# Kernel tuning notes

Measured on AMD Instinct MI355X. Metric: run time of the kernel, lower is better.

The kernel has to match this reference:

```python
import jax, jax.numpy as jnp
import numpy as np

B = 8192
D_LS, D_A, D_LM, D_AT, D_DS, D_DM = 1024, 512, 512, 512, 1024, 512
LENGTH = D_LS + D_A + D_LM  # 2048
OUT = 512


def setup_inputs() -> dict:
    key = jax.random.key(0)
    ks = jax.random.split(key, 9)
    return {
        "result_ls": jax.random.normal(ks[0], (B, 1, D_LS), jnp.float32),
        "result_A": jax.random.normal(ks[1], (B, 1, D_A), jnp.float32),
        "result_lm": jax.random.normal(ks[2], (B, 1, D_LM), jnp.float32),
        "result_AT": jax.random.normal(ks[3], (B, 1, D_AT), jnp.float32),
        "result_ds": jax.random.normal(ks[4], (B, 1, D_DS), jnp.float32),
        "result_dm": jax.random.normal(ks[5], (B, 1, D_DM), jnp.float32),
        "W": jax.random.normal(ks[6], (OUT, LENGTH), jnp.float32) * (1.0 / np.sqrt(LENGTH)),
        "b": jax.random.normal(ks[7], (OUT,), jnp.float32) * 0.01,
        "h_n": jax.random.normal(ks[8], (OUT, 1), jnp.float32) * (1.0 / np.sqrt(OUT)),
    }


def _pad_to(x, length):
    # zero-pad last dim of [B,1,d] to [B,1,length]
    return jnp.pad(x, ((0, 0), (0, 0), (0, length - x.shape[2])))


def reference(result_ls, result_A, result_lm, result_AT, result_ds, result_dm, W, b, h_n):
    # pad each node-type feature to common length and stack along node axis -> [B,6,L]
    nodes = jnp.concatenate(
        [_pad_to(t, LENGTH) for t in (result_ls, result_A, result_lm, result_AT, result_ds, result_dm)],
        axis=1,
    )
    temp = jnp.tanh(jnp.einsum("bnl,ol->bno", nodes, W) + b)  # [B,6,OUT]
    score = jnp.einsum("bno,oi->bni", temp, h_n)               # [B,6,1]
    score = score.reshape(-1, 1, 6)
    beta = jax.nn.softmax(score, axis=2)                        # [B,1,6]
    z_i = jnp.matmul(beta, nodes)                               # [B,1,L]
    return z_i
```

## Files before the change

### kernel.cpp

```cpp
#include <hip/hip_runtime.h>
#include <hip/hip_bf16.h>
#include <stdint.h>

typedef __attribute__((ext_vector_type(8))) short bf16x8;
typedef __attribute__((ext_vector_type(4))) float f32x4;

#define NB 8192

__device__ __forceinline__ unsigned pkbf(float x, float y) {
    __hip_bfloat162 h = __float22bfloat162_rn(make_float2(x, y));
    unsigned r;
    __builtin_memcpy(&r, &h, 4);
    return r;
}

__device__ __forceinline__ uint4 pack8(float4 a, float4 b) {
    uint4 r;
    r.x = pkbf(a.x, a.y);
    r.y = pkbf(a.z, a.w);
    r.z = pkbf(b.x, b.y);
    r.w = pkbf(b.z, b.w);
    return r;
}

__device__ __forceinline__ void gload_lds16(const float* g, void* l) {
    __builtin_amdgcn_global_load_lds(
        (const __attribute__((address_space(1))) void*)g,
        (__attribute__((address_space(3))) void*)l, 16, 0, 0);
}

__global__ __launch_bounds__(256)
void prep_w_kernel(const float* __restrict__ W, uint4* __restrict__ Wt) {
    int t = blockIdx.x * 256 + threadIdx.x;
    int lane = t & 63;
    int frag = t >> 6;
    int kb = frag >> 5, cb = frag & 31;
    int o = cb * 16 + (lane & 15);
    int k = kb * 32 + ((lane >> 4) << 3);
    const float* src = W + (size_t)o * 2048 + k;
    float4 a = *(const float4*)src;
    float4 b = *(const float4*)(src + 4);
    Wt[t] = pack8(a, b);
}

__global__ __launch_bounds__(512, 4)
void score_kernel(const float* __restrict__ x0, const float* __restrict__ x1,
                  const float* __restrict__ x2, const float* __restrict__ x3,
                  const float* __restrict__ x4, const float* __restrict__ x5,
                  const float* __restrict__ bias, const float* __restrict__ hvec,
                  const uint4* __restrict__ Wt, float* __restrict__ scores) {
    __shared__ uint4 lA[2][1024];
    __shared__ float red[8][64];

    int bid = blockIdx.x;
    int node = bid % 6;
    int tile = bid / 6;
    const float* xp; int dn;
    switch (node) {
        case 0: xp = x0; dn = 1024; break;
        case 1: xp = x1; dn = 512;  break;
        case 2: xp = x2; dn = 512;  break;
        case 3: xp = x3; dn = 512;  break;
        case 4: xp = x4; dn = 1024; break;
        default: xp = x5; dn = 512; break;
    }
    int m0 = tile * 64;
    int t = threadIdx.x;
    int lane = t & 63;
    int w = t >> 6;

    int nst = dn >> 6;

    int ra = ((w << 1) + 0) * 4 + (lane >> 4);
    int rb = ((w << 1) + 1) * 4 + (lane >> 4);
    int sa = (lane & 15) ^ (ra & 7);
    int sb = (lane & 15) ^ (rb & 7);
    const float* ga = xp + (size_t)(m0 + ra) * dn + (sa << 2);
    const float* gb = xp + (size_t)(m0 + rb) * dn + (sb << 2);
    char* lbaseA = (char*)&lA[0][0] + (((w << 1) + 0) << 10);
    char* lbaseB = (char*)&lA[0][0] + (((w << 1) + 1) << 10);

    gload_lds16(ga, lbaseA);
    gload_lds16(gb, lbaseB);
    ga += 64; gb += 64;
    __syncthreads();

    f32x4 acc[4][4];
#pragma unroll
    for (int mf = 0; mf < 4; ++mf)
#pragma unroll
        for (int nf = 0; nf < 4; ++nf)
            acc[mf][nf] = (f32x4){0.f, 0.f, 0.f, 0.f};

    const char* ldsroot = (const char*)&lA[0][0];

    for (int s = 0; s < nst; ++s) {
        int cur = s & 1;
        if (s + 1 < nst) {
            gload_lds16(ga, lbaseA + ((cur ^ 1) << 14));
            gload_lds16(gb, lbaseB + ((cur ^ 1) << 14));
            ga += 64; gb += 64;
        }
#pragma unroll
        for (int ks = 0; ks < 2; ++ks) {
            int kblock = (s << 1) + ks;
            const uint4* wp = Wt + (((kblock << 5) + (w << 2)) << 6) + lane;
            bf16x8 bfr[4];
#pragma unroll
            for (int nf = 0; nf < 4; ++nf) {
                uint4 u = wp[nf << 6];
                __builtin_memcpy(&bfr[nf], &u, 16);
            }
#pragma unroll
            for (int mf = 0; mf < 4; ++mf) {
                int r = (mf << 4) + (lane & 15);
                int slot = (ks << 3) + ((lane >> 4) << 1);
                int sw = r & 7;
                const char* p = ldsroot + (cur << 14) + (r << 8);
                float4 lo = *(const float4*)(p + (((slot) ^ sw) << 4));
                float4 hi = *(const float4*)(p + (((slot + 1) ^ sw) << 4));
                uint4 pk = pack8(lo, hi);
                bf16x8 afr;
                __builtin_memcpy(&afr, &pk, 16);
#pragma unroll
                for (int nf = 0; nf < 4; ++nf)
                    acc[mf][nf] = __builtin_amdgcn_mfma_f32_16x16x32_bf16(
                        afr, bfr[nf], acc[mf][nf], 0, 0, 0);
            }
        }
        __syncthreads();
    }

    float bv[4], hv[4];
#pragma unroll
    for (int nf = 0; nf < 4; ++nf) {
        int o = (w << 6) + (nf << 4) + (lane & 15);
        bv[nf] = bias[o];
        hv[nf] = hvec[o];
    }
#pragma unroll
    for (int mf = 0; mf < 4; ++mf) {
        float sc[4] = {0.f, 0.f, 0.f, 0.f};
#pragma unroll
        for (int nf = 0; nf < 4; ++nf) {
#pragma unroll
            for (int r = 0; r < 4; ++r) {
                float xv = acc[mf][nf][r] + bv[nf];
                float th = 1.f - 2.f * __builtin_amdgcn_rcpf(1.f + __expf(2.f * xv));
                sc[r] = fmaf(hv[nf], th, sc[r]);
            }
        }
#pragma unroll
        for (int r = 0; r < 4; ++r) {
            float v = sc[r];
            v += __shfl_xor(v, 1);
            v += __shfl_xor(v, 2);
            v += __shfl_xor(v, 4);
            v += __shfl_xor(v, 8);
            if ((lane & 15) == 0)
                red[w][(mf << 4) + ((lane >> 4) << 2) + r] = v;
        }
    }
    __syncthreads();
    if (t < 64) {
        float ssum = 0.f;
#pragma unroll
        for (int w2 = 0; w2 < 8; ++w2) ssum += red[w2][t];
        scores[node * NB + m0 + t] = ssum;
    }
}

__global__ __launch_bounds__(256)
void z_kernel(const float* __restrict__ x0, const float* __restrict__ x1,
              const float* __restrict__ x2, const float* __restrict__ x3,
              const float* __restrict__ x4, const float* __restrict__ x5,
              const float* __restrict__ scores, float* __restrict__ out) {
    int wv = threadIdx.x >> 6;
    int lane = threadIdx.x & 63;
    int b = (blockIdx.x << 2) + wv;

    float s0 = scores[b];
    float s1 = scores[NB + b];
    float s2 = scores[2 * NB + b];
    float s3 = scores[3 * NB + b];
    float s4 = scores[4 * NB + b];
    float s5 = scores[5 * NB + b];
    float m = fmaxf(fmaxf(fmaxf(s0, s1), fmaxf(s2, s3)), fmaxf(s4, s5));
    float e0 = __expf(s0 - m), e1 = __expf(s1 - m), e2 = __expf(s2 - m);
    float e3 = __expf(s3 - m), e4 = __expf(s4 - m), e5 = __expf(s5 - m);
    float inv = __builtin_amdgcn_rcpf(e0 + e1 + e2 + e3 + e4 + e5);
    float b0 = e0 * inv, b1 = e1 * inv, b2 = e2 * inv;
    float b3 = e3 * inv, b4 = e4 * inv, b5 = e5 * inv;

    const float* pls = x0 + (size_t)b * 1024;
    const float* pA  = x1 + (size_t)b * 512;
    const float* plm = x2 + (size_t)b * 512;
    const float* pAT = x3 + (size_t)b * 512;
    const float* pds = x4 + (size_t)b * 1024;
    const float* pdm = x5 + (size_t)b * 512;
    float* po = out + (size_t)b * 2048;

#pragma unroll
    for (int j = 0; j < 2; ++j) {
        int c = (j << 8) + (lane << 2);
        float4 vls = *(const float4*)(pls + c);
        float4 vA  = *(const float4*)(pA + c);
        float4 vlm = *(const float4*)(plm + c);
        float4 vAT = *(const float4*)(pAT + c);
        float4 vds = *(const float4*)(pds + c);
        float4 vdm = *(const float4*)(pdm + c);
        float4 r;
        r.x = b0*vls.x + b1*vA.x + b2*vlm.x + b3*vAT.x + b4*vds.x + b5*vdm.x;
        r.y = b0*vls.y + b1*vA.y + b2*vlm.y + b3*vAT.y + b4*vds.y + b5*vdm.y;
        r.z = b0*vls.z + b1*vA.z + b2*vlm.z + b3*vAT.z + b4*vds.z + b5*vdm.z;
        r.w = b0*vls.w + b1*vA.w + b2*vlm.w + b3*vAT.w + b4*vds.w + b5*vdm.w;
        *(float4*)(po + c) = r;
    }
#pragma unroll
    for (int j = 0; j < 2; ++j) {
        int c = 512 + (j << 8) + (lane << 2);
        float4 vls = *(const float4*)(pls + c);
        float4 vds = *(const float4*)(pds + c);
        float4 r;
        r.x = b0*vls.x + b4*vds.x;
        r.y = b0*vls.y + b4*vds.y;
        r.z = b0*vls.z + b4*vds.z;
        r.w = b0*vls.w + b4*vds.w;
        *(float4*)(po + c) = r;
    }
    float4 zz = make_float4(0.f, 0.f, 0.f, 0.f);
#pragma unroll
    for (int j = 0; j < 4; ++j) {
        int c = 1024 + (j << 8) + (lane << 2);
        *(float4*)(po + c) = zz;
    }
}

extern "C" void kernel_launch(void* const* d_in, const int* in_sizes, int n_in,
                              void* d_out, int out_size, void* d_ws, size_t ws_size,
                              hipStream_t stream) {
    const float* x0   = (const float*)d_in[0];
    const float* x1   = (const float*)d_in[1];
    const float* x2   = (const float*)d_in[2];
    const float* x3   = (const float*)d_in[3];
    const float* x4   = (const float*)d_in[4];
    const float* x5   = (const float*)d_in[5];
    const float* W    = (const float*)d_in[6];
    const float* bias = (const float*)d_in[7];
    const float* hvec = (const float*)d_in[8];

    uint4* Wt = (uint4*)d_ws;
    float* scores = (float*)((char*)d_ws + (1u << 20));

    prep_w_kernel<<<256, 256, 0, stream>>>(W, Wt);
    score_kernel<<<768, 512, 0, stream>>>(x0, x1, x2, x3, x4, x5, bias, hvec, Wt, scores);
    z_kernel<<<2048, 256, 0, stream>>>(x0, x1, x2, x3, x4, x5, scores, (float*)d_out);
}
```

Baseline: 114.0 us.

## Template score kernel per node depth, pre-pack activations to bf16 in LDS

Splits the score GEMM into two templated launches: the 1024-wide nodes use 64-row tiles, and the 512-wide nodes use 128-row tiles so each W fragment load is reused across more rows. Activations are now read with register loads and converted to bf16 fragment layout once before being stored to LDS, replacing the async global-to-LDS fp32 copies and the per-MFMA LDS repacking. This removes repeated conversion work and halves LDS traffic per stage. The cost is more registers and a lower occupancy bound, and the global loads are no longer asynchronous into LDS.

After: 101.5 us. 1.12x faster.

```diff
diff --git a/kernel.cpp b/kernel.cpp
--- a/kernel.cpp
+++ b/kernel.cpp
@@ -21,12 +21,6 @@
     r.z = pkbf(b.x, b.y);
     r.w = pkbf(b.z, b.w);
     return r;
-}
-
-__device__ __forceinline__ void gload_lds16(const float* g, void* l) {
-    __builtin_amdgcn_global_load_lds(
-        (const __attribute__((address_space(1))) void*)g,
-        (__attribute__((address_space(3))) void*)l, 16, 0, 0);
 }
 
 __global__ __launch_bounds__(256)
@@ -43,90 +37,102 @@
     Wt[t] = pack8(a, b);
 }
 
-__global__ __launch_bounds__(512, 4)
-void score_kernel(const float* __restrict__ x0, const float* __restrict__ x1,
-                  const float* __restrict__ x2, const float* __restrict__ x3,
-                  const float* __restrict__ x4, const float* __restrict__ x5,
+template<int MFN, int DN, int NN>
+__global__ __launch_bounds__(512, 2)
+void score_kernel(const float* __restrict__ p0, const float* __restrict__ p1,
+                  const float* __restrict__ p2, const float* __restrict__ p3,
+                  int n0, int n1, int n2, int n3,
                   const float* __restrict__ bias, const float* __restrict__ hvec,
                   const uint4* __restrict__ Wt, float* __restrict__ scores) {
-    __shared__ uint4 lA[2][1024];
-    __shared__ float red[8][64];
+    constexpr int BM = MFN * 16;
+    constexpr int NST = DN / 64;
+    constexpr int FRAGS = 2 * MFN;
+
+    __shared__ uint4 lA[2][FRAGS * 64];
+    __shared__ float red[8][BM];
 
     int bid = blockIdx.x;
-    int node = bid % 6;
-    int tile = bid / 6;
-    const float* xp; int dn;
-    switch (node) {
-        case 0: xp = x0; dn = 1024; break;
-        case 1: xp = x1; dn = 512;  break;
-        case 2: xp = x2; dn = 512;  break;
-        case 3: xp = x3; dn = 512;  break;
-        case 4: xp = x4; dn = 1024; break;
-        default: xp = x5; dn = 512; break;
-    }
-    int m0 = tile * 64;
+    int ni = bid % NN;
+    int tile = bid / NN;
+    const float* xp; int node;
+    switch (ni) {
+        case 0: xp = p0; node = n0; break;
+        case 1: xp = p1; node = n1; break;
+        case 2: xp = p2; node = n2; break;
+        default: xp = p3; node = n3; break;
+    }
+    int m0 = tile * BM;
     int t = threadIdx.x;
-    int lane = t & 63;
+    int l = t & 63;
     int w = t >> 6;
 
-    int nst = dn >> 6;
-
-    int ra = ((w << 1) + 0) * 4 + (lane >> 4);
-    int rb = ((w << 1) + 1) * 4 + (lane >> 4);
-    int sa = (lane & 15) ^ (ra & 7);
-    int sb = (lane & 15) ^ (rb & 7);
-    const float* ga = xp + (size_t)(m0 + ra) * dn + (sa << 2);
-    const float* gb = xp + (size_t)(m0 + rb) * dn + (sb << 2);
-    char* lbaseA = (char*)&lA[0][0] + (((w << 1) + 0) << 10);
-    char* lbaseB = (char*)&lA[0][0] + (((w << 1) + 1) << 10);
-
-    gload_lds16(ga, lbaseA);
-    gload_lds16(gb, lbaseB);
-    ga += 64; gb += 64;
+    int cf = t >> 6;
+    int r1 = (cf % MFN) * 16 + (l & 15);
+    int k1 = (cf / MFN) * 32 + ((l >> 4) << 3);
+    const float* g1 = xp + (size_t)(m0 + r1) * DN + k1;
+    const float* g2 = g1 + 32;
+
+    {
+        float4 a0 = *(const float4*)g1;
+        float4 a1 = *(const float4*)(g1 + 4);
+        lA[0][t] = pack8(a0, a1);
+        if constexpr (MFN == 8) {
+            float4 b0 = *(const float4*)g2;
+            float4 b1 = *(const float4*)(g2 + 4);
+            lA[0][t + 512] = pack8(b0, b1);
+        }
+    }
     __syncthreads();
 
-    f32x4 acc[4][4];
-#pragma unroll
-    for (int mf = 0; mf < 4; ++mf)
+    f32x4 acc[MFN][4];
+#pragma unroll
+    for (int mf = 0; mf < MFN; ++mf)
 #pragma unroll
         for (int nf = 0; nf < 4; ++nf)
             acc[mf][nf] = (f32x4){0.f, 0.f, 0.f, 0.f};
 
-    const char* ldsroot = (const char*)&lA[0][0];
-
-    for (int s = 0; s < nst; ++s) {
+    for (int s = 0; s < NST; ++s) {
         int cur = s & 1;
-        if (s + 1 < nst) {
-            gload_lds16(ga, lbaseA + ((cur ^ 1) << 14));
-            gload_lds16(gb, lbaseB + ((cur ^ 1) << 14));
-            ga += 64; gb += 64;
-        }
+        float4 a0, a1, b0, b1;
+        bool hn = (s + 1) < NST;
+        if (hn) {
+            const float* q = g1 + (s + 1) * 64;
+            a0 = *(const float4*)q;
+            a1 = *(const float4*)(q + 4);
+            if constexpr (MFN == 8) {
+                const float* q2 = g2 + (s + 1) * 64;
+                b0 = *(const float4*)q2;
+                b1 = *(const float4*)(q2 + 4);
+            }
+        }
+        bf16x8 bfr[2][4];
 #pragma unroll
         for (int ks = 0; ks < 2; ++ks) {
-            int kblock = (s << 1) + ks;
-            const uint4* wp = Wt + (((kblock << 5) + (w << 2)) << 6) + lane;
-            bf16x8 bfr[4];
+            int kb = (s << 1) + ks;
+            const uint4* wp = Wt + (((kb << 5) + (w << 2)) << 6) + l;
 #pragma unroll
             for (int nf = 0; nf < 4; ++nf) {
                 uint4 u = wp[nf << 6];
-                __builtin_memcpy(&bfr[nf], &u, 16);
-            }
-#pragma unroll
-            for (int mf = 0; mf < 4; ++mf) {
-                int r = (mf << 4) + (lane & 15);
-                int slot = (ks << 3) + ((lane >> 4) << 1);
-                int sw = r & 7;
-                const char* p = ldsroot + (cur << 14) + (r << 8);
-                float4 lo = *(const float4*)(p + (((slot) ^ sw) << 4));
-                float4 hi = *(const float4*)(p + (((slot + 1) ^ sw) << 4));
-                uint4 pk = pack8(lo, hi);
+                __builtin_memcpy(&bfr[ks][nf], &u, 16);
+            }
+        }
+#pragma unroll
+        for (int ks = 0; ks < 2; ++ks) {
+#pragma unroll
+            for (int mf = 0; mf < MFN; ++mf) {
+                uint4 u = lA[cur][(ks * MFN + mf) * 64 + l];
                 bf16x8 afr;
-                __builtin_memcpy(&afr, &pk, 16);
+                __builtin_memcpy(&afr, &u, 16);
 #pragma unroll
                 for (int nf = 0; nf < 4; ++nf)
                     acc[mf][nf] = __builtin_amdgcn_mfma_f32_16x16x32_bf16(
-                        afr, bfr[nf], acc[mf][nf], 0, 0, 0);
-            }
+                        afr, bfr[ks][nf], acc[mf][nf], 0, 0, 0);
+            }
+        }
+        if (hn) {
+            lA[cur ^ 1][t] = pack8(a0, a1);
+            if constexpr (MFN == 8)
+                lA[cur ^ 1][t + 512] = pack8(b0, b1);
         }
         __syncthreads();
     }
@@ -134,12 +140,12 @@
     float bv[4], hv[4];
 #pragma unroll
     for (int nf = 0; nf < 4; ++nf) {
-        int o = (w << 6) + (nf << 4) + (lane & 15);
+        int o = (w << 6) + (nf << 4) + (l & 15);
         bv[nf] = bias[o];
         hv[nf] = hvec[o];
     }
 #pragma unroll
-    for (int mf = 0; mf < 4; ++mf) {
+    for (int mf = 0; mf < MFN; ++mf) {
         float sc[4] = {0.f, 0.f, 0.f, 0.f};
 #pragma unroll
         for (int nf = 0; nf < 4; ++nf) {
@@ -157,12 +163,12 @@
             v += __shfl_xor(v, 2);
             v += __shfl_xor(v, 4);
             v += __shfl_xor(v, 8);
-            if ((lane & 15) == 0)
-                red[w][(mf << 4) + ((lane >> 4) << 2) + r] = v;
+            if ((l & 15) == 0)
+                red[w][(mf << 4) + ((l >> 4) << 2) + r] = v;
         }
     }
     __syncthreads();
-    if (t < 64) {
+    if (t < BM) {
         float ssum = 0.f;
 #pragma unroll
         for (int w2 = 0; w2 < 8; ++w2) ssum += red[w2][t];
@@ -253,6 +259,9 @@
     float* scores = (float*)((char*)d_ws + (1u << 20));
 
     prep_w_kernel<<<256, 256, 0, stream>>>(W, Wt);
-    score_kernel<<<768, 512, 0, stream>>>(x0, x1, x2, x3, x4, x5, bias, hvec, Wt, scores);
+    score_kernel<4, 1024, 2><<<256, 512, 0, stream>>>(
+        x0, x4, x0, x4, 0, 4, 0, 4, bias, hvec, Wt, scores);
+    score_kernel<8, 512, 4><<<256, 512, 0, stream>>>(
+        x1, x2, x3, x5, 1, 2, 3, 5, bias, hvec, Wt, scores);
     z_kernel<<<2048, 256, 0, stream>>>(x0, x1, x2, x3, x4, x5, scores, (float*)d_out);
 }
```

## Convert activations to bf16 at load time and widen per-wave output tile in score kernel

Applied to the files above, without the earlier changes.

The score kernel now uses 256 threads with 4 waves, and each wave covers 128 output columns (8 MFMA n-fragments) instead of 64. That doubles B-fragment reuse per A fragment and halves the number of waves that re-read the same activations. Activations are loaded into registers, packed to bf16 in MFMA fragment order and stored to LDS, replacing the async global_load_lds fp32 path with its swizzled LDS reads and per-use conversion. The next-tile loads are issued before the MFMAs, and the LDS writes follow them. Costs are higher register pressure (the 4x8 accumulators plus 16 B-fragments) and fewer waves per block, which may lower occupancy and latency hiding.

Result: slower. 118.1 us (+3.6%).

```diff
diff --git a/kernel.cpp b/kernel.cpp
--- a/kernel.cpp
+++ b/kernel.cpp
@@ -21,12 +21,6 @@
     r.z = pkbf(b.x, b.y);
     r.w = pkbf(b.z, b.w);
     return r;
-}
-
-__device__ __forceinline__ void gload_lds16(const float* g, void* l) {
-    __builtin_amdgcn_global_load_lds(
-        (const __attribute__((address_space(1))) void*)g,
-        (__attribute__((address_space(3))) void*)l, 16, 0, 0);
 }
 
 __global__ __launch_bounds__(256)
@@ -43,14 +37,14 @@
     Wt[t] = pack8(a, b);
 }
 
-__global__ __launch_bounds__(512, 4)
+__global__ __launch_bounds__(256, 2)
 void score_kernel(const float* __restrict__ x0, const float* __restrict__ x1,
                   const float* __restrict__ x2, const float* __restrict__ x3,
                   const float* __restrict__ x4, const float* __restrict__ x5,
                   const float* __restrict__ bias, const float* __restrict__ hvec,
                   const uint4* __restrict__ Wt, float* __restrict__ scores) {
-    __shared__ uint4 lA[2][1024];
-    __shared__ float red[8][64];
+    __shared__ uint4 lA[2][512];
+    __shared__ float red[4][64];
 
     int bid = blockIdx.x;
     int node = bid % 6;
@@ -66,75 +60,79 @@
     }
     int m0 = tile * 64;
     int t = threadIdx.x;
-    int lane = t & 63;
+    int l = t & 63;
     int w = t >> 6;
 
     int nst = dn >> 6;
 
-    int ra = ((w << 1) + 0) * 4 + (lane >> 4);
-    int rb = ((w << 1) + 1) * 4 + (lane >> 4);
-    int sa = (lane & 15) ^ (ra & 7);
-    int sb = (lane & 15) ^ (rb & 7);
-    const float* ga = xp + (size_t)(m0 + ra) * dn + (sa << 2);
-    const float* gb = xp + (size_t)(m0 + rb) * dn + (sb << 2);
-    char* lbaseA = (char*)&lA[0][0] + (((w << 1) + 0) << 10);
-    char* lbaseB = (char*)&lA[0][0] + (((w << 1) + 1) << 10);
-
-    gload_lds16(ga, lbaseA);
-    gload_lds16(gb, lbaseB);
-    ga += 64; gb += 64;
+    int srow = (t >> 6) * 16 + (l & 15);
+    const float* g1 = xp + (size_t)(m0 + srow) * dn + ((l >> 4) << 3);
+    const float* g2 = g1 + 32;
+
+    {
+        float4 a0 = *(const float4*)g1;
+        float4 a1 = *(const float4*)(g1 + 4);
+        float4 c0 = *(const float4*)g2;
+        float4 c1 = *(const float4*)(g2 + 4);
+        lA[0][t] = pack8(a0, a1);
+        lA[0][t + 256] = pack8(c0, c1);
+    }
     __syncthreads();
 
-    f32x4 acc[4][4];
+    f32x4 acc[4][8];
 #pragma unroll
     for (int mf = 0; mf < 4; ++mf)
 #pragma unroll
-        for (int nf = 0; nf < 4; ++nf)
+        for (int nf = 0; nf < 8; ++nf)
             acc[mf][nf] = (f32x4){0.f, 0.f, 0.f, 0.f};
-
-    const char* ldsroot = (const char*)&lA[0][0];
 
     for (int s = 0; s < nst; ++s) {
         int cur = s & 1;
-        if (s + 1 < nst) {
-            gload_lds16(ga, lbaseA + ((cur ^ 1) << 14));
-            gload_lds16(gb, lbaseB + ((cur ^ 1) << 14));
-            ga += 64; gb += 64;
-        }
+        float4 a0, a1, c0, c1;
+        bool hn = (s + 1) < nst;
+        if (hn) {
+            const float* q = g1 + (s + 1) * 64;
+            a0 = *(const float4*)q;
+            a1 = *(const float4*)(q + 4);
+            const float* q2 = g2 + (s + 1) * 64;
+            c0 = *(const float4*)q2;
+            c1 = *(const float4*)(q2 + 4);
+        }
+        bf16x8 bfr[2][8];
 #pragma unroll
         for (int ks = 0; ks < 2; ++ks) {
-            int kblock = (s << 1) + ks;
-            const uint4* wp = Wt + (((kblock << 5) + (w << 2)) << 6) + lane;
-            bf16x8 bfr[4];
-#pragma unroll
-            for (int nf = 0; nf < 4; ++nf) {
+            int kb = (s << 1) + ks;
+            const uint4* wp = Wt + (((kb << 5) + (w << 3)) << 6) + l;
+#pragma unroll
+            for (int nf = 0; nf < 8; ++nf) {
                 uint4 u = wp[nf << 6];
-                __builtin_memcpy(&bfr[nf], &u, 16);
+                __builtin_memcpy(&bfr[ks][nf], &u, 16);
             }
+        }
+#pragma unroll
+        for (int ks = 0; ks < 2; ++ks) {
 #pragma unroll
             for (int mf = 0; mf < 4; ++mf) {
-                int r = (mf << 4) + (lane & 15);
-                int slot = (ks << 3) + ((lane >> 4) << 1);
-                int sw = r & 7;
-                const char* p = ldsroot + (cur << 14) + (r << 8);
-                float4 lo = *(const float4*)(p + (((slot) ^ sw) << 4));
-                float4 hi = *(const float4*)(p + (((slot + 1) ^ sw) << 4));
-                uint4 pk = pack8(lo, hi);
+                uint4 u = lA[cur][((ks << 2) + mf) * 64 + l];
                 bf16x8 afr;
-                __builtin_memcpy(&afr, &pk, 16);
-#pragma unroll
-                for (int nf = 0; nf < 4; ++nf)
+                __builtin_memcpy(&afr, &u, 16);
+#pragma unroll
+                for (int nf = 0; nf < 8; ++nf)
                     acc[mf][nf] = __builtin_amdgcn_mfma_f32_16x16x32_bf16(
-                        afr, bfr[nf], acc[mf][nf], 0, 0, 0);
+                        afr, bfr[ks][nf], acc[mf][nf], 0, 0, 0);
             }
         }
+        if (hn) {
+            lA[cur ^ 1][t] = pack8(a0, a1);
+            lA[cur ^ 1][t + 256] = pack8(c0, c1);
+        }
         __syncthreads();
     }
 
-    float bv[4], hv[4];
-#pragma unroll
-    for (int nf = 0; nf < 4; ++nf) {
-        int o = (w << 6) + (nf << 4) + (lane & 15);
+    float bv[8], hv[8];
+#pragma unroll
+    for (int nf = 0; nf < 8; ++nf) {
+        int o = (w << 7) + (nf << 4) + (l & 15);
         bv[nf] = bias[o];
         hv[nf] = hvec[o];
     }
@@ -142,7 +140,7 @@
     for (int mf = 0; mf < 4; ++mf) {
         float sc[4] = {0.f, 0.f, 0.f, 0.f};
 #pragma unroll
-        for (int nf = 0; nf < 4; ++nf) {
+        for (int nf = 0; nf < 8; ++nf) {
 #pragma unroll
             for (int r = 0; r < 4; ++r) {
                 float xv = acc[mf][nf][r] + bv[nf];
@@ -157,15 +155,13 @@
             v += __shfl_xor(v, 2);
             v += __shfl_xor(v, 4);
             v += __shfl_xor(v, 8);
-            if ((lane & 15) == 0)
-                red[w][(mf << 4) + ((lane >> 4) << 2) + r] = v;
+            if ((l & 15) == 0)
+                red[w][(mf << 4) + ((l >> 4) << 2) + r] = v;
         }
     }
     __syncthreads();
     if (t < 64) {
-        float ssum = 0.f;
-#pragma unroll
-        for (int w2 = 0; w2 < 8; ++w2) ssum += red[w2][t];
+        float ssum = red[0][t] + red[1][t] + red[2][t] + red[3][t];
         scores[node * NB + m0 + t] = ssum;
     }
 }
@@ -253,6 +249,6 @@
     float* scores = (float*)((char*)d_ws + (1u << 20));
 
     prep_w_kernel<<<256, 256, 0, stream>>>(W, Wt);
-    score_kernel<<<768, 512, 0, stream>>>(x0, x1, x2, x3, x4, x5, bias, hvec, Wt, scores);
+    score_kernel<<<768, 256, 0, stream>>>(x0, x1, x2, x3, x4, x5, bias, hvec, Wt, scores);
     z_kernel<<<2048, 256, 0, stream>>>(x0, x1, x2, x3, x4, x5, scores, (float*)d_out);
 }
```
